# Performance work log

Measured on AMD Instinct MI355X. Metric: run time of the kernel, lower is better.

The kernel has to match this reference:

```python
import jax, jax.numpy as jnp
import numpy as np

N = 50000          # num_nodes
E = 800000         # num_edges (avg degree 16)
HID = 128          # hidden_dim
NH = 8             # num_heads
HD = 16            # head_dim
FFN = 512          # ffn_dim
EPS = 1e-5


def setup_inputs() -> dict:
    key = jax.random.key(0)
    ks = jax.random.split(key, 12)
    s = 0.02
    d = {}
    d["x"] = jax.random.normal(ks[0], (N, HID), jnp.float32)
    d["edge_index"] = jax.random.randint(ks[1], (2, E), 0, N, dtype=jnp.int32)
    # projection weights stored as [in, out] (math identical to torch Linear)
    d["Wq"] = jax.random.normal(ks[2], (HID, NH * HD), jnp.float32) * s
    d["bq"] = jnp.zeros((NH * HD,), jnp.float32)
    d["Wk"] = jax.random.normal(ks[3], (HID, NH * HD), jnp.float32) * s
    d["bk"] = jnp.zeros((NH * HD,), jnp.float32)
    d["Wv"] = jax.random.normal(ks[4], (HID, NH * HD), jnp.float32) * s
    d["bv"] = jnp.zeros((NH * HD,), jnp.float32)
    d["Wo"] = jax.random.normal(ks[5], (NH * HD, HID), jnp.float32) * s
    d["bo"] = jnp.zeros((HID,), jnp.float32)
    d["g1"] = jnp.ones((HID,), jnp.float32)
    d["b1"] = jnp.zeros((HID,), jnp.float32)
    d["g2"] = jnp.ones((HID,), jnp.float32)
    d["b2"] = jnp.zeros((HID,), jnp.float32)
    d["W1"] = jax.random.normal(ks[6], (HID, FFN), jnp.float32) * s
    d["bf1"] = jnp.zeros((FFN,), jnp.float32)
    d["W2"] = jax.random.normal(ks[7], (FFN, HID), jnp.float32) * s
    d["bf2"] = jnp.zeros((HID,), jnp.float32)
    return d


def _layer_norm(x, g, b):
    m = jnp.mean(x, axis=-1, keepdims=True)
    v = jnp.mean((x - m) ** 2, axis=-1, keepdims=True)
    return (x - m) * jax.lax.rsqrt(v + EPS) * g + b


def _gnn_layer(x, edge_index, Wq, bq, Wk, bk, Wv, bv, Wo, bo,
               g1, b1, g2, b2, W1, bf1, W2, bf2):
    n = x.shape[0]
    residual = x
    h = _layer_norm(x, g1, b1)

    q = (h @ Wq + bq).reshape(n, NH, HD)
    k = (h @ Wk + bk).reshape(n, NH, HD)
    v = (h @ Wv + bv).reshape(n, NH, HD)

    src, dst = edge_index[0], edge_index[1]
    # original code skips nodes with no in-neighbors (output stays zero)
    deg = jax.ops.segment_sum(jnp.ones(src.shape, x.dtype), dst, num_segments=n)
    # self-loop appended for every attended node
    loops = jnp.arange(n, dtype=src.dtype)
    s_all = jnp.concatenate([src, loops])
    d_all = jnp.concatenate([dst, loops])

    # edge-parallel scaled dot-product scores: [E+N, NH]
    e = jnp.sum(q[d_all] * k[s_all], axis=-1) / np.sqrt(HD).astype(np.float32)
    m = jax.lax.stop_gradient(jax.ops.segment_max(e, d_all, num_segments=n))
    p = jnp.exp(e - m[d_all])
    z = jax.ops.segment_sum(p, d_all, num_segments=n)
    alpha = p / z[d_all]                                   # segment softmax
    agg = jax.ops.segment_sum(alpha[:, :, None] * v[s_all], d_all,
                              num_segments=n)              # [n, NH, HD]
    agg = jnp.where(deg[:, None, None] > 0, agg, jnp.zeros_like(agg))

    att = agg.reshape(n, NH * HD) @ Wo + bo
    x = residual + att                                     # dropout=0 (eval)

    residual = x
    h = _layer_norm(x, g2, b2)
    ffn = jax.nn.gelu(h @ W1 + bf1, approximate=False) @ W2 + bf2
    return residual + ffn


def reference(x, edge_index, Wq, bq, Wk, bk, Wv, bv, Wo, bo,
              g1, b1, g2, b2, W1, bf1, W2, bf2):
    return _gnn_layer(x, edge_index, Wq, bq, Wk, bk, Wv, bv, Wo, bo,
                      g1, b1, g2, b2, W1, bf1, W2, bf2)
```

## Files before the change

### kernel.cpp

```cpp
#include <hip/hip_runtime.h>
#include <hip/hip_bf16.h>

typedef __hip_bfloat16 bf16;
typedef __attribute__((ext_vector_type(8))) short s16x8;
typedef __attribute__((ext_vector_type(4))) float f32x4;

__device__ __forceinline__ float2 bfpair(unsigned u) {
    float2 r;
    r.x = __uint_as_float(u << 16);
    r.y = __uint_as_float(u & 0xffff0000u);
    return r;
}

__device__ __forceinline__ unsigned short f2bf_bits(float f) {
    unsigned u = __float_as_uint(f);
    return (unsigned short)((u + 0x7fffu + ((u >> 16) & 1u)) >> 16);
}

typedef const __attribute__((address_space(1))) unsigned GU;
typedef __attribute__((address_space(3))) unsigned LU;
__device__ __forceinline__ void gload_lds16(const void* g, void* l) {
    __builtin_amdgcn_global_load_lds((GU*)g, (LU*)l, 16, 0, 0);
}

__global__ __launch_bounds__(256) void setup_k(const float* __restrict__ Wq,
                                               const float* __restrict__ Wk,
                                               const float* __restrict__ Wv,
                                               const float* __restrict__ Wo,
                                               const float* __restrict__ W1,
                                               const float* __restrict__ W2,
                                               const float* __restrict__ bq,
                                               const float* __restrict__ bk,
                                               const float* __restrict__ bv,
                                               unsigned short* __restrict__ qkvH,
                                               unsigned short* __restrict__ woH,
                                               unsigned short* __restrict__ w1H,
                                               unsigned short* __restrict__ w2H,
                                               float* __restrict__ bqkv,
                                               int* __restrict__ deg,
                                               const unsigned* __restrict__ eisrc,
                                               int* __restrict__ ei32,
                                               const float* __restrict__ x,
                                               const float* __restrict__ g1,
                                               const float* __restrict__ b1,
                                               bf16* __restrict__ hb,
                                               int N, int twoE, int nzero) {
    int b = blockIdx.x;
    int tid = threadIdx.x;
    if (b < 770) {
        int idx = b * 256 + tid;
        if (idx >= 196608) {
            int i = idx - 196608;
            if (i < 384) bqkv[i] = (i < 128) ? bq[i] : (i < 256) ? bk[i - 128] : bv[i - 256];
            return;
        }
        float w; unsigned short *H; int oi;
        if (idx < 49152) {
            int n = idx >> 7, kx = idx & 127;
            const float* W = (n < 128) ? Wq : (n < 256) ? Wk : Wv;
            w = W[kx * 128 + (n & 127)];
            H = qkvH; oi = idx;
        } else if (idx < 65536) {
            int li = idx - 49152; int n = li >> 7, kx = li & 127;
            w = Wo[kx * 128 + n]; H = woH; oi = li;
        } else if (idx < 131072) {
            int li = idx - 65536; int n = li >> 7, kx = li & 127;
            w = W1[(size_t)kx * 512 + n]; H = w1H; oi = li;
        } else {
            int li = idx - 131072; int n = li >> 9, kx = li & 511;
            w = W2[(size_t)kx * 128 + n]; H = w2H; oi = li;
        }
        H[oi] = f2bf_bits(w);
        return;
    }
    if (b < 770 + nzero) {
        int i = (b - 770) * 256 + tid;
        if (i < N) deg[i] = 0;
        return;
    }
    if (b < 770 + nzero + 2000) {
        __shared__ int s_nz;
        if (tid == 0) s_nz = 0;
        __syncthreads();
        if (eisrc[2 * tid + 1] != 0u) atomicAdd(&s_nz, 1);
        __syncthreads();
        bool is64 = (s_nz == 0);
        long long i = (long long)(b - 770 - nzero) * 256 + tid;
        long long st = (long long)2000 * 256;
        if (is64) { for (; i < twoE; i += st) ei32[i] = (int)eisrc[2 * i]; }
        else      { for (; i < twoE; i += st) ei32[i] = (int)eisrc[i]; }
        return;
    }
    int row = (b - 770 - nzero - 2000) * 4 + (tid >> 6);
    if (row >= N) return;
    int lane = tid & 63;
    float2 f = ((const float2*)x)[(size_t)row * 64 + lane];
    float s = f.x + f.y;
    #pragma unroll
    for (int off = 32; off > 0; off >>= 1) s += __shfl_xor(s, off);
    float mean = s * (1.0f / 128.0f);
    float d0 = f.x - mean, d1 = f.y - mean;
    float vs = d0 * d0 + d1 * d1;
    #pragma unroll
    for (int off = 32; off > 0; off >>= 1) vs += __shfl_xor(vs, off);
    float rstd = rsqrtf(vs * (1.0f / 128.0f) + 1e-5f);
    float2 gg = ((const float2*)g1)[lane];
    float2 bb = ((const float2*)b1)[lane];
    float o0 = d0 * rstd * gg.x + bb.x;
    float o1 = d1 * rstd * gg.y + bb.y;
    unsigned pk = ((unsigned)f2bf_bits(o1) << 16) | (unsigned)f2bf_bits(o0);
    ((unsigned*)hb)[(size_t)row * 64 + lane] = pk;
}

__global__ __launch_bounds__(256) void count_deg_k(const int* __restrict__ ei,
                                                   int* __restrict__ deg, int E) {
    int e = blockIdx.x * 256 + threadIdx.x;
    if (e < E) atomicAdd(&deg[ei[E + e]], 1);
}

#define SCAN_BLK 1024
__global__ __launch_bounds__(256) void scan1_k(const int* __restrict__ deg,
                                               int* __restrict__ off,
                                               int* __restrict__ bsum, int n) {
    __shared__ int s[256];
    int base = blockIdx.x * SCAN_BLK;
    int t = threadIdx.x;
    int v[4]; int sum = 0;
    #pragma unroll
    for (int j = 0; j < 4; j++) {
        int idx = base + t * 4 + j;
        v[j] = (idx < n) ? deg[idx] : 0;
        sum += v[j];
    }
    s[t] = sum; __syncthreads();
    for (int o = 1; o < 256; o <<= 1) {
        int add = (t >= o) ? s[t - o] : 0;
        __syncthreads();
        s[t] += add;
        __syncthreads();
    }
    int run = (t > 0) ? s[t - 1] : 0;
    if (t == 255) bsum[blockIdx.x] = s[255];
    #pragma unroll
    for (int j = 0; j < 4; j++) {
        int idx = base + t * 4 + j;
        if (idx < n) off[idx] = run;
        run += v[j];
    }
}

__global__ __launch_bounds__(256) void scan3_k(int* __restrict__ off,
                                               int* __restrict__ cursor,
                                               const int* __restrict__ bsum,
                                               int n, int nb) {
    __shared__ int sb[64];
    int t = threadIdx.x;
    if (t < 64) {
        int own = (t < nb) ? bsum[t] : 0;
        int v = own;
        #pragma unroll
        for (int o = 1; o < 64; o <<= 1) {
            int u = __shfl_up(v, o);
            if ((t & 63) >= o) v += u;
        }
        sb[t] = v - own;
    }
    __syncthreads();
    int i = blockIdx.x * 256 + t;
    if (i < n) {
        int o = off[i] + sb[i / SCAN_BLK];
        off[i] = o;
        cursor[i] = o;
    }
}

__global__ __launch_bounds__(256) void scatter_k(const int* __restrict__ ei,
                                                 int* __restrict__ cursor,
                                                 int* __restrict__ csr, int E) {
    int e = blockIdx.x * 256 + threadIdx.x;
    if (e >= E) return;
    int s = ei[e], d = ei[E + e];
    int pos = atomicAdd(&cursor[d], 1);
    csr[pos] = s;
}

template <int EPI, bool OUTBF, int K, int BM, bool LNF>
__global__ __launch_bounds__(256) void mgemm_k(const bf16* __restrict__ A,
                                               const bf16* __restrict__ Bh,
                                               const float* __restrict__ bias,
                                               const float* __restrict__ res,
                                               void* __restrict__ outp,
                                               const float* __restrict__ lg,
                                               const float* __restrict__ lb,
                                               bf16* __restrict__ hbout,
                                               long long sub_off, int M,
                                               int ldo, int sub_shift) {
    constexpr int MF = BM / 32;
    constexpr int NK = K / 32;
    constexpr int STEP = BM * 64 + 8192;
    __shared__ __align__(16) char smem[2 * STEP];

    const int nwg = gridDim.x * gridDim.y;
    const int orig = blockIdx.y * gridDim.x + blockIdx.x;
    const int qq = nwg >> 3, rr = nwg & 7;
    const int xcd = orig & 7, jj = orig >> 3;
    const int tile = ((xcd < rr) ? xcd * (qq + 1) : rr * (qq + 1) + (xcd - rr) * qq) + jj;
    const int bx = tile % gridDim.x;
    const int by = tile / gridDim.x;

    const int lane = threadIdx.x & 63;
    const int wid  = threadIdx.x >> 6;
    const int wr = wid >> 1, wc = wid & 1;
    const int lrow = lane & 15, lk = lane >> 4;
    const int m0 = by * BM;
    const int mw0 = wr * (BM / 2);
    const int n0 = bx * 128 + wc * 64;
    const int srow = lane >> 2;
    const int schunk = (lane & 3) ^ ((srow >> 1) & 3);

    const char* Ab  = (const char*)A  + (size_t)m0 * (K * 2);
    const char* Bhb = (const char*)Bh + (size_t)(bx * 128) * (K * 2);

    f32x4 acc[MF][4];
    #pragma unroll
    for (int mf = 0; mf < MF; mf++)
        #pragma unroll
        for (int nf = 0; nf < 4; nf++) {
            f32x4 z = {0.f, 0.f, 0.f, 0.f};
            acc[mf][nf] = z;
        }

    auto stage = [&](int kt, int bufb) {
        const int kb = kt * 64;
        char* sb = &smem[bufb];
        #pragma unroll
        for (int it = 0; it < BM / 64; it++) {
            int rg = wid * (BM / 4) + it * 16;
            gload_lds16(Ab + (size_t)(rg + srow) * (K * 2) + kb + schunk * 16,
                        sb + rg * 64);
        }
        #pragma unroll
        for (int it = 0; it < 2; it++) {
            int rg = wid * 32 + it * 16;
            gload_lds16(Bhb + (size_t)(rg + srow) * (K * 2) + kb + schunk * 16,
                        sb + BM * 64 + rg * 64);
        }
    };

    auto compute = [&](int bufb) {
        const char* sb = &smem[bufb];
        s16x8 a[MF], bh[4];
        #pragma unroll
        for (int mf = 0; mf < MF; mf++) {
            int ra = mw0 + mf * 16 + lrow;
            a[mf] = *(const s16x8*)(sb + ra * 64 + ((lk ^ ((ra >> 1) & 3)) * 16));
        }
        #pragma unroll
        for (int nf = 0; nf < 4; nf++) {
            int rb = wc * 64 + nf * 16 + lrow;
            int co = (lk ^ ((rb >> 1) & 3)) * 16;
            bh[nf] = *(const s16x8*)(sb + BM * 64 + rb * 64 + co);
        }
        #pragma unroll
        for (int mf = 0; mf < MF; mf++)
            #pragma unroll
            for (int nf = 0; nf < 4; nf++)
                acc[mf][nf] = __builtin_amdgcn_mfma_f32_16x16x32_bf16(a[mf], bh[nf], acc[mf][nf], 0, 0, 0);
    };

    stage(0, 0);
    for (int kt = 0; kt < NK; kt++) {
        __syncthreads();
        if (kt + 1 < NK) stage(kt + 1, ((kt + 1) & 1) * STEP);
        compute((kt & 1) * STEP);
    }

    if (!LNF) {
        const int nmask = (1 << sub_shift) - 1;
        #pragma unroll
        for (int mf = 0; mf < MF; mf++) {
            #pragma unroll
            for (int nf = 0; nf < 4; nf++) {
                int n = n0 + nf * 16 + lrow;
                float bsv = bias[n];
                #pragma unroll
                for (int r = 0; r < 4; r++) {
                    int m = m0 + mw0 + mf * 16 + lk * 4 + r;
                    if (m >= M) continue;
                    float val = acc[mf][nf][r] + bsv;
                    if (EPI == 1) val = 0.5f * val * (1.0f + erff(val * 0.70710678118f));
                    if (EPI == 2) val += res[(size_t)m * ldo + n];
                    long long oidx = (long long)m * ldo + (n & nmask) + (long long)(n >> sub_shift) * sub_off;
                    if (OUTBF) ((unsigned short*)outp)[oidx] = f2bf_bits(val);
                    else       ((float*)outp)[oidx] = val;
                }
            }
        }
    } else {
        float vals[MF][4][4];
        float s1[MF][4], s2[MF][4];
        #pragma unroll
        for (int mf = 0; mf < MF; mf++)
            #pragma unroll
            for (int r = 0; r < 4; r++) { s1[mf][r] = 0.f; s2[mf][r] = 0.f; }
        #pragma unroll
        for (int mf = 0; mf < MF; mf++) {
            #pragma unroll
            for (int r = 0; r < 4; r++) {
                int m = m0 + mw0 + mf * 16 + lk * 4 + r;
                #pragma unroll
                for (int nf = 0; nf < 4; nf++) {
                    int n = n0 + nf * 16 + lrow;
                    float val = acc[mf][nf][r] + bias[n];
                    val += (m < M) ? res[(size_t)m * 128 + n] : 0.f;
                    vals[mf][nf][r] = val;
                    s1[mf][r] += val;
                    s2[mf][r] += val * val;
                }
                #pragma unroll
                for (int o = 1; o < 16; o <<= 1) {
                    s1[mf][r] += __shfl_xor(s1[mf][r], o);
                    s2[mf][r] += __shfl_xor(s2[mf][r], o);
                }
            }
        }
        float2* lns = (float2*)smem;
        __syncthreads();
        if (lrow == 0) {
            #pragma unroll
            for (int mf = 0; mf < MF; mf++)
                #pragma unroll
                for (int r = 0; r < 4; r++) {
                    int rl = mw0 + mf * 16 + lk * 4 + r;
                    float2 p; p.x = s1[mf][r]; p.y = s2[mf][r];
                    lns[rl * 2 + wc] = p;
                }
        }
        __syncthreads();
        #pragma unroll
        for (int mf = 0; mf < MF; mf++) {
            #pragma unroll
            for (int r = 0; r < 4; r++) {
                int rl = mw0 + mf * 16 + lk * 4 + r;
                int m = m0 + rl;
                float2 pa = lns[rl * 2 + 0], pb = lns[rl * 2 + 1];
                float mean = (pa.x + pb.x) * (1.0f / 128.0f);
                float var  = (pa.y + pb.y) * (1.0f / 128.0f) - mean * mean;
                float rstd = rsqrtf(var + 1e-5f);
                if (m >= M) continue;
                #pragma unroll
                for (int nf = 0; nf < 4; nf++) {
                    int n = n0 + nf * 16 + lrow;
                    float val = vals[mf][nf][r];
                    ((float*)outp)[(size_t)m * 128 + n] = val;
                    float o = (val - mean) * rstd * lg[n] + lb[n];
                    ((unsigned short*)hbout)[(size_t)m * 128 + n] = f2bf_bits(o);
                }
            }
        }
    }
}

__global__ __launch_bounds__(256) void node_agg_k(const bf16* __restrict__ q,
                                                  const bf16* __restrict__ k,
                                                  const bf16* __restrict__ v,
                                                  const int* __restrict__ off,
                                                  const int* __restrict__ deg,
                                                  const int* __restrict__ csr,
                                                  bf16* __restrict__ agg, int NN) {
    int node = blockIdx.x * 4 + (threadIdx.x >> 6);
    if (node >= NN) return;
    int lane = threadIdx.x & 63;
    float2 qf = bfpair(((const unsigned*)(q + (size_t)node * 128))[lane]);
    int start = off[node];
    int cnt = deg[node];
    float acc0 = 0.f, acc1 = 0.f, zsum = 0.f;
    if (cnt < 64) {
        int T = cnt + 1;
        int s_vec = (lane < cnt) ? csr[start + lane] : node;
        for (int e0 = 0; e0 < T; e0 += 8) {
            unsigned ku[8], vu[8];
            #pragma unroll
            for (int j = 0; j < 8; j++) {
                if (e0 + j < T) {
                    int s = __shfl(s_vec, e0 + j);
                    ku[j] = ((const unsigned*)(k + (size_t)s * 128))[lane];
                    vu[j] = ((const unsigned*)(v + (size_t)s * 128))[lane];
                }
            }
            #pragma unroll
            for (int j = 0; j < 8; j++) {
                if (e0 + j < T) {
                    float2 kf = bfpair(ku[j]);
                    float dot = qf.x * kf.x + qf.y * kf.y;
                    dot += __shfl_xor(dot, 1);
                    dot += __shfl_xor(dot, 2);
                    dot += __shfl_xor(dot, 4);
                    float p = __expf(dot * 0.25f);
                    zsum += p;
                    float2 vf = bfpair(vu[j]);
                    acc0 += p * vf.x;
                    acc1 += p * vf.y;
                }
            }
        }
    } else {
        for (int e = 0; e <= cnt; e++) {
            int s = (e < cnt) ? csr[start + e] : node;
            float2 kf = bfpair(((const unsigned*)(k + (size_t)s * 128))[lane]);
            float dot = qf.x * kf.x + qf.y * kf.y;
            dot += __shfl_xor(dot, 1);
            dot += __shfl_xor(dot, 2);
            dot += __shfl_xor(dot, 4);
            float p = __expf(dot * 0.25f);
            zsum += p;
            float2 vf = bfpair(((const unsigned*)(v + (size_t)s * 128))[lane]);
            acc0 += p * vf.x;
            acc1 += p * vf.y;
        }
    }
    float2 o;
    if (cnt == 0) { o.x = 0.f; o.y = 0.f; }
    else { float inv = 1.0f / zsum; o.x = acc0 * inv; o.y = acc1 * inv; }
    unsigned pk = ((unsigned)f2bf_bits(o.y) << 16) | (unsigned)f2bf_bits(o.x);
    ((unsigned*)agg)[(size_t)node * 64 + lane] = pk;
}

extern "C" void kernel_launch(void* const* d_in, const int* in_sizes, int n_in,
                              void* d_out, int out_size, void* d_ws, size_t ws_size,
                              hipStream_t stream) {
    const float* x  = (const float*)d_in[0];
    const void*  eiRaw = d_in[1];
    const float* Wq = (const float*)d_in[2];
    const float* bq = (const float*)d_in[3];
    const float* Wk = (const float*)d_in[4];
    const float* bk = (const float*)d_in[5];
    const float* Wv = (const float*)d_in[6];
    const float* bv = (const float*)d_in[7];
    const float* Wo = (const float*)d_in[8];
    const float* bo = (const float*)d_in[9];
    const float* g1 = (const float*)d_in[10];
    const float* b1 = (const float*)d_in[11];
    const float* g2 = (const float*)d_in[12];
    const float* b2 = (const float*)d_in[13];
    const float* W1 = (const float*)d_in[14];
    const float* bf1 = (const float*)d_in[15];
    const float* W2 = (const float*)d_in[16];
    const float* bf2 = (const float*)d_in[17];
    float* out = (float*)d_out;

    const int N = in_sizes[0] / 128;
    const int E = in_sizes[1] / 2;
    const int gy = (N + 127) / 128;
    const int gy64 = (N + 63) / 64;
    const int Mp = gy * 128;

    char* w = (char*)d_ws;
    size_t off_b = 0;
    auto alloc = [&](size_t bytes) -> void* {
        void* ptr = w + off_b;
        off_b = (off_b + bytes + 255) & ~(size_t)255;
        return ptr;
    };
    int*   deg    = (int*)alloc((size_t)N * 4);
    int*   offA   = (int*)alloc((size_t)N * 4);
    int*   cursor = (int*)alloc((size_t)N * 4);
    int*   bsum   = (int*)alloc(64 * 4);
    int*   ei32   = (int*)alloc((size_t)E * 2 * 4);
    int*   csr    = (int*)alloc((size_t)E * 4);
    bf16*  hb     = (bf16*)alloc((size_t)Mp * 128 * 2);
    bf16*  qkvb   = (bf16*)alloc((size_t)N * 3 * 128 * 2);
    bf16*  aggb   = (bf16*)alloc((size_t)Mp * 128 * 2);
    bf16*  t      = (bf16*)alloc((size_t)Mp * 512 * 2);
    unsigned short* qkvH = (unsigned short*)alloc(49152 * 2);
    unsigned short* woH  = (unsigned short*)alloc(16384 * 2);
    unsigned short* w1H  = (unsigned short*)alloc(65536 * 2);
    unsigned short* w2H  = (unsigned short*)alloc(65536 * 2);
    float* bqkv = (float*)alloc(384 * 4);
    (void)ws_size; (void)n_in; (void)out_size;

    int nb = (N + SCAN_BLK - 1) / SCAN_BLK;
    int nzero = (N + 255) / 256;
    int lnb = (N + 3) / 4;

    setup_k<<<770 + nzero + 2000 + lnb, 256, 0, stream>>>(
        Wq, Wk, Wv, Wo, W1, W2, bq, bk, bv,
        qkvH, woH, w1H, w2H, bqkv,
        deg, (const unsigned*)eiRaw, ei32, x, g1, b1, hb, N, E * 2, nzero);
    count_deg_k<<<(E + 255) / 256, 256, 0, stream>>>(ei32, deg, E);
    scan1_k<<<nb, 256, 0, stream>>>(deg, offA, bsum, N);
    scan3_k<<<(N + 255) / 256, 256, 0, stream>>>(offA, cursor, bsum, N, nb);
    scatter_k<<<(E + 255) / 256, 256, 0, stream>>>(ei32, cursor, csr, E);

    bf16* qb = qkvb;
    bf16* kb = qkvb + (size_t)N * 128;
    bf16* vb = qkvb + (size_t)N * 256;

    mgemm_k<0, true, 128, 128, false><<<dim3(3, gy), 256, 0, stream>>>(
        hb, (const bf16*)qkvH, bqkv, nullptr, qkvb,
        nullptr, nullptr, nullptr, (long long)N * 128, N, 128, 7);
    node_agg_k<<<(N + 3) / 4, 256, 0, stream>>>(qb, kb, vb, offA, deg, csr, aggb, N);
    mgemm_k<2, false, 128, 64, true><<<dim3(1, gy64), 256, 0, stream>>>(
        aggb, (const bf16*)woH, bo, x, out,
        g2, b2, hb, 0, N, 128, 15);
    mgemm_k<1, true, 128, 128, false><<<dim3(4, gy), 256, 0, stream>>>(
        hb, (const bf16*)w1H, bf1, nullptr, t,
        nullptr, nullptr, nullptr, 0, N, 512, 15);
    mgemm_k<2, false, 512, 64, false><<<dim3(1, gy64), 256, 0, stream>>>(
        t, (const bf16*)w2H, bf2, out, out,
        nullptr, nullptr, nullptr, 0, N, 128, 15);
}
```

Baseline: 383.3 us.

## Fuse FFN up-projection, GELU and down-projection into one kernel

Replaces the two FFN GEMM launches with a single kernel that, per 64-row tile, loops over eight 64-wide chunks of the hidden FFN dimension. Each chunk computes h·W1 plus bias and GELU into LDS, then immediately multiplies by the matching W2 slice into register accumulators. This removes the global round-trip of the N×512 bf16 intermediate and one launch. In exchange, W1 and W2 are re-staged per block without double buffering, which adds barriers and may lower MFMA utilisation; LDS use is 56KB per block.

```diff
diff --git a/kernel.cpp b/kernel.cpp
--- a/kernel.cpp
+++ b/kernel.cpp
@@ -361,6 +361,158 @@
     }
 }
 
+__global__ __launch_bounds__(256) void ffn_k(const bf16* __restrict__ hb,
+                                             const bf16* __restrict__ w1,
+                                             const bf16* __restrict__ w2,
+                                             const float* __restrict__ bf1,
+                                             const float* __restrict__ bf2,
+                                             float* __restrict__ out, int M) {
+    __shared__ __align__(16) char smem[57344];
+    char* sA  = smem;
+    char* sW1 = smem + 16384;
+    char* sW2 = smem + 32768;
+    char* sMT = smem + 49152;
+
+    const int nwg = gridDim.x;
+    const int orig = blockIdx.x;
+    const int qq = nwg >> 3, rr = nwg & 7;
+    const int xcd = orig & 7, jj = orig >> 3;
+    const int by = ((xcd < rr) ? xcd * (qq + 1) : rr * (qq + 1) + (xcd - rr) * qq) + jj;
+
+    const int lane = threadIdx.x & 63;
+    const int wid  = threadIdx.x >> 6;
+    const int wr = wid >> 1, wc = wid & 1;
+    const int lrow = lane & 15, lk = lane >> 4;
+    const int m0 = by * 64;
+    const int srow = lane >> 2;
+    const int schunk = (lane & 3) ^ ((srow >> 1) & 3);
+
+    const char* Ab = (const char*)hb + (size_t)m0 * 256;
+
+    #pragma unroll
+    for (int ks = 0; ks < 4; ks++) {
+        int rg = wid * 16;
+        gload_lds16(Ab + (size_t)(rg + srow) * 256 + ks * 64 + schunk * 16,
+                    sA + ks * 4096 + rg * 64);
+    }
+
+    auto stageW = [&](int fc) {
+        const char* W1b = (const char*)w1 + (size_t)(fc * 64) * 256;
+        #pragma unroll
+        for (int ks = 0; ks < 4; ks++) {
+            int rg = wid * 16;
+            gload_lds16(W1b + (size_t)(rg + srow) * 256 + ks * 64 + schunk * 16,
+                        sW1 + ks * 4096 + rg * 64);
+        }
+        const char* W2b = (const char*)w2 + (size_t)(fc * 64) * 2;
+        #pragma unroll
+        for (int ks = 0; ks < 2; ks++) {
+            #pragma unroll
+            for (int it = 0; it < 2; it++) {
+                int rg = wid * 32 + it * 16;
+                gload_lds16(W2b + (size_t)(rg + srow) * 1024 + ks * 64 + schunk * 16,
+                            sW2 + ks * 8192 + rg * 64);
+            }
+        }
+    };
+
+    f32x4 oacc[2][4];
+    #pragma unroll
+    for (int mf = 0; mf < 2; mf++)
+        #pragma unroll
+        for (int nf = 0; nf < 4; nf++) {
+            f32x4 z = {0.f, 0.f, 0.f, 0.f};
+            oacc[mf][nf] = z;
+        }
+
+    stageW(0);
+    for (int fc = 0; fc < 8; fc++) {
+        __syncthreads();
+        f32x4 macc[2][2];
+        #pragma unroll
+        for (int mf = 0; mf < 2; mf++)
+            #pragma unroll
+            for (int nf = 0; nf < 2; nf++) {
+                f32x4 z = {0.f, 0.f, 0.f, 0.f};
+                macc[mf][nf] = z;
+            }
+        #pragma unroll
+        for (int ks = 0; ks < 4; ks++) {
+            s16x8 a[2], bw[2];
+            #pragma unroll
+            for (int mf = 0; mf < 2; mf++) {
+                int ra = wr * 32 + mf * 16 + lrow;
+                a[mf] = *(const s16x8*)(sA + ks * 4096 + ra * 64 + ((lk ^ ((ra >> 1) & 3)) * 16));
+            }
+            #pragma unroll
+            for (int nf = 0; nf < 2; nf++) {
+                int rf = wc * 32 + nf * 16 + lrow;
+                bw[nf] = *(const s16x8*)(sW1 + ks * 4096 + rf * 64 + ((lk ^ ((rf >> 1) & 3)) * 16));
+            }
+            #pragma unroll
+            for (int mf = 0; mf < 2; mf++)
+                #pragma unroll
+                for (int nf = 0; nf < 2; nf++)
+                    macc[mf][nf] = __builtin_amdgcn_mfma_f32_16x16x32_bf16(a[mf], bw[nf], macc[mf][nf], 0, 0, 0);
+        }
+        #pragma unroll
+        for (int mf = 0; mf < 2; mf++) {
+            #pragma unroll
+            for (int nf = 0; nf < 2; nf++) {
+                int f = wc * 32 + nf * 16 + lrow;
+                float bv = bf1[fc * 64 + f];
+                #pragma unroll
+                for (int r = 0; r < 4; r++) {
+                    int m = wr * 32 + mf * 16 + lk * 4 + r;
+                    float val = macc[mf][nf][r] + bv;
+                    val = 0.5f * val * (1.0f + erff(val * 0.70710678118f));
+                    int byte = m * 128 + (((f >> 3) ^ (m & 7)) * 16) + (f & 7) * 2;
+                    *(unsigned short*)(sMT + byte) = f2bf_bits(val);
+                }
+            }
+        }
+        __syncthreads();
+        #pragma unroll
+        for (int ks = 0; ks < 2; ks++) {
+            s16x8 a2[2], b2[4];
+            #pragma unroll
+            for (int mf = 0; mf < 2; mf++) {
+                int ra = wr * 32 + mf * 16 + lrow;
+                int fch = ks * 4 + lk;
+                a2[mf] = *(const s16x8*)(sMT + ra * 128 + ((fch ^ (ra & 7)) * 16));
+            }
+            #pragma unroll
+            for (int nf = 0; nf < 4; nf++) {
+                int rb = wc * 64 + nf * 16 + lrow;
+                b2[nf] = *(const s16x8*)(sW2 + ks * 8192 + rb * 64 + ((lk ^ ((rb >> 1) & 3)) * 16));
+            }
+            #pragma unroll
+            for (int mf = 0; mf < 2; mf++)
+                #pragma unroll
+                for (int nf = 0; nf < 4; nf++)
+                    oacc[mf][nf] = __builtin_amdgcn_mfma_f32_16x16x32_bf16(a2[mf], b2[nf], oacc[mf][nf], 0, 0, 0);
+        }
+        __syncthreads();
+        if (fc + 1 < 8) stageW(fc + 1);
+    }
+
+    #pragma unroll
+    for (int mf = 0; mf < 2; mf++) {
+        #pragma unroll
+        for (int nf = 0; nf < 4; nf++) {
+            int n = wc * 64 + nf * 16 + lrow;
+            float bsv = bf2[n];
+            #pragma unroll
+            for (int r = 0; r < 4; r++) {
+                int m = m0 + wr * 32 + mf * 16 + lk * 4 + r;
+                if (m >= M) continue;
+                float val = oacc[mf][nf][r] + bsv + out[(size_t)m * 128 + n];
+                out[(size_t)m * 128 + n] = val;
+            }
+        }
+    }
+}
+
 __global__ __launch_bounds__(256) void node_agg_k(const bf16* __restrict__ q,
                                                   const bf16* __restrict__ k,
                                                   const bf16* __restrict__ v,
@@ -471,7 +623,6 @@
     bf16*  hb     = (bf16*)alloc((size_t)Mp * 128 * 2);
     bf16*  qkvb   = (bf16*)alloc((size_t)N * 3 * 128 * 2);
     bf16*  aggb   = (bf16*)alloc((size_t)Mp * 128 * 2);
-    bf16*  t      = (bf16*)alloc((size_t)Mp * 512 * 2);
     unsigned short* qkvH = (unsigned short*)alloc(49152 * 2);
     unsigned short* woH  = (unsigned short*)alloc(16384 * 2);
     unsigned short* w1H  = (unsigned short*)alloc(65536 * 2);
@@ -503,10 +654,6 @@
     mgemm_k<2, false, 128, 64, true><<<dim3(1, gy64), 256, 0, stream>>>(
         aggb, (const bf16*)woH, bo, x, out,
         g2, b2, hb, 0, N, 128, 15);
-    mgemm_k<1, true, 128, 128, false><<<dim3(4, gy), 256, 0, stream>>>(
-        hb, (const bf16*)w1H, bf1, nullptr, t,
-        nullptr, nullptr, nullptr, 0, N, 512, 15);
-    mgemm_k<2, false, 512, 64, false><<<dim3(1, gy64), 256, 0, stream>>>(
-        t, (const bf16*)w2H, bf2, out, out,
-        nullptr, nullptr, nullptr, 0, N, 128, 15);
-}
+    ffn_k<<<gy64, 256, 0, stream>>>(hb, (const bf16*)w1H, (const bf16*)w2H,
+                                    bf1, bf2, out, N);
+}
```

Result: faster. 370.0 us (-3.5%).
